# Kernel tuning notes

Hardware: AMD Instinct MI355X
Metric: run time of the kernel (lower is better)

The kernel has to match this reference:

```python
import jax, jax.numpy as jnp
import numpy as np
import math

B, L, H, NH, DH = 2, 2048, 1024, 16, 64  # batch, seq, hidden, heads, head dim


def setup_inputs() -> dict:
    key = jax.random.key(0)
    ks = jax.random.split(key, 12)
    s = 0.02
    return {
        "v": jax.random.normal(ks[0], (B, L, H), jnp.float32),
        "k": jax.random.normal(ks[1], (B, L, H), jnp.float32),
        "q": jax.random.normal(ks[2], (B, L, H), jnp.float32),
        "mask": jnp.zeros((B, 1, 1, L), jnp.bool_),
        "Wv": jax.random.normal(ks[3], (H, H), jnp.float32) * s,
        "bv": jnp.zeros((H,), jnp.float32),
        "Wk": jax.random.normal(ks[4], (H, H), jnp.float32) * s,
        "bk": jnp.zeros((H,), jnp.float32),
        "Wq": jax.random.normal(ks[5], (H, H), jnp.float32) * s,
        "bq": jnp.zeros((H,), jnp.float32),
        "Wt": jax.random.normal(ks[6], (H, 1), jnp.float32) * s,
        "bt": jnp.zeros((1,), jnp.float32),
        "Wm": jax.random.normal(ks[7], (H, H), jnp.float32) * s,
        "bm": jnp.zeros((H,), jnp.float32),
    }


def reference(v, k, q, mask, Wv, bv, Wk, bk, Wq, bq, Wt, bt, Wm, bm):
    vp = (v @ Wv + bv).reshape(B, L, NH, DH).transpose(0, 2, 1, 3)  # [B,NH,L,DH]
    kp = k @ Wk + bk  # [B,L,H]
    qp = q @ Wq + bq  # [B,L,H]
    threshold = (qp * kp) @ Wt + bt  # [B,L,1] learned per-position gate threshold
    kh = kp.reshape(B, L, NH, DH).transpose(0, 2, 1, 3)  # [B,NH,L,DH]
    qh = qp.reshape(B, L, NH, DH).transpose(0, 2, 1, 3)
    scores = jnp.einsum("bhqd,bhkd->bhqk", qh, kh) / math.sqrt(DH)
    scores = jnp.where(mask, -1e9, scores)
    att_map = jax.nn.softmax(scores, axis=-1)  # [B,NH,Lq,Lk]
    # column sums: over queries (axis -2) then over heads -> [B,Lk,1]
    colsum = att_map.sum(axis=2).sum(axis=1)[..., None]
    a = (colsum - threshold) > 0  # [B,L,1] boolean gate
    atted = jnp.einsum("bhqk,bhkd->bhqd", att_map, vp)  # [B,NH,L,DH]
    atted = atted.transpose(0, 2, 1, 3).reshape(B, L, H)
    atted = atted * a.astype(atted.dtype)
    return atted @ Wm + bm
```

## Files before the change

### kernel.cpp

```cpp
#include <hip/hip_runtime.h>
#include <math.h>

#define BATCH 2
#define SEQ   2048
#define HID   1024
#define NHEAD 16
#define DHEAD 64
#define MROWS (BATCH*SEQ)
#define QK_SCALE 0.125f

typedef __attribute__((ext_vector_type(8))) short short8;
typedef __attribute__((ext_vector_type(4))) short short4v;
typedef __attribute__((ext_vector_type(4))) float floatx4;
#define MFMA16(a,b,c) __builtin_amdgcn_mfma_f32_16x16x32_bf16(a,b,c,0,0,0)

__device__ __forceinline__ unsigned short f2bf(float x) {
    union { float f; unsigned u; } v; v.f = x;
    return (unsigned short)((v.u + 0x8000u) >> 16);
}
__device__ __forceinline__ float bf2f(unsigned short s) {
    union { unsigned u; float f; } v; v.u = ((unsigned)s) << 16;
    return v.f;
}
__device__ __forceinline__ unsigned pack_bf16(float lo, float hi) {
    union { float f; unsigned u; } a, b; a.f = lo; b.f = hi;
    return __builtin_amdgcn_perm(b.u + 0x8000u, a.u + 0x8000u, 0x07060302u);
}

__global__ __launch_bounds__(256) void cvt_bf16_kernel(
    const float* __restrict__ i0, const float* __restrict__ i1,
    const float* __restrict__ i2,
    unsigned short* __restrict__ o0, unsigned short* __restrict__ o1,
    unsigned short* __restrict__ o2)
{
    const float* in; unsigned short* out;
    switch (blockIdx.y) {
        case 0:  in = i0; out = o0; break;
        case 1:  in = i1; out = o1; break;
        default: in = i2; out = o2; break;
    }
    const size_t i = ((size_t)blockIdx.x * 256 + threadIdx.x) * 8;
    const float4 a = *(const float4*)&in[i];
    const float4 b = *(const float4*)&in[i + 4];
    uint4 u;
    u.x = pack_bf16(a.x, a.y); u.y = pack_bf16(a.z, a.w);
    u.z = pack_bf16(b.x, b.y); u.w = pack_bf16(b.z, b.w);
    *(uint4*)&out[i] = u;
}

__global__ __launch_bounds__(256) void wtrans_kernel(
    const float* __restrict__ W0, const float* __restrict__ W1,
    const float* __restrict__ W2, const float* __restrict__ W3,
    unsigned short* __restrict__ T0, unsigned short* __restrict__ T1,
    unsigned short* __restrict__ T2, unsigned short* __restrict__ T3)
{
    const float* W; unsigned short* Wt;
    switch (blockIdx.z) {
        case 0: W = W0; Wt = T0; break;
        case 1: W = W1; Wt = T1; break;
        case 2: W = W2; Wt = T2; break;
        default: W = W3; Wt = T3; break;
    }
    __shared__ float T[64][68];
    const int tid = threadIdx.x;
    const int k0 = blockIdx.x * 64, n0 = blockIdx.y * 64;
#pragma unroll
    for (int it = 0; it < 4; it++) {
        const int id = it * 256 + tid;
        const int r = id >> 4, c4 = (id & 15) << 2;
        *(float4*)&T[r][c4] = *(const float4*)&W[(size_t)(k0 + r) * HID + n0 + c4];
    }
    __syncthreads();
#pragma unroll
    for (int it = 0; it < 2; it++) {
        const int id = it * 256 + tid;
        const int n = id >> 3, k8 = (id & 7) << 3;
        uint4 u;
        u.x = pack_bf16(T[k8 + 0][n], T[k8 + 1][n]);
        u.y = pack_bf16(T[k8 + 2][n], T[k8 + 3][n]);
        u.z = pack_bf16(T[k8 + 4][n], T[k8 + 5][n]);
        u.w = pack_bf16(T[k8 + 6][n], T[k8 + 7][n]);
        *(uint4*)&Wt[(size_t)(n0 + n) * HID + k0 + k8] = u;
    }
}

__global__ __launch_bounds__(256) void vtrans_kernel(
    const unsigned short* __restrict__ vb, unsigned short* __restrict__ vt)
{
    __shared__ unsigned short T[64][72];
    const int b = blockIdx.z, h = blockIdx.y, l0 = blockIdx.x * 64;
    const int tid = threadIdx.x;
#pragma unroll
    for (int it = 0; it < 2; it++) {
        const int id = it * 256 + tid;
        const int l = id >> 3, c8 = (id & 7) << 3;
        *(uint4*)&T[l][c8] =
            *(const uint4*)&vb[(size_t)(b * SEQ + l0 + l) * HID + h * DHEAD + c8];
    }
    __syncthreads();
#pragma unroll
    for (int it = 0; it < 2; it++) {
        const int id = it * 256 + tid;
        const int d = id >> 3, l8 = (id & 7) << 3;
        ushort4 u0, u1;
        u0.x = T[l8 + 0][d]; u0.y = T[l8 + 1][d];
        u0.z = T[l8 + 2][d]; u0.w = T[l8 + 3][d];
        u1.x = T[l8 + 4][d]; u1.y = T[l8 + 5][d];
        u1.z = T[l8 + 6][d]; u1.w = T[l8 + 7][d];
        const size_t o = ((size_t)(b * NHEAD + h) * DHEAD + d) * SEQ + l0 + l8;
        *(ushort4*)&vt[o] = u0;
        *(ushort4*)&vt[o + 4] = u1;
    }
}

__global__ __launch_bounds__(256) void gemm_mfma_kernel(
    const unsigned short* __restrict__ Ab, const unsigned short* __restrict__ Bt,
    const float* __restrict__ bias,
    const float* __restrict__ gate_cs, const float* __restrict__ gate_th,
    float* __restrict__ Cf, unsigned short* __restrict__ Cb,
    int M, int N, int K)
{
    __shared__ unsigned short As[128][72];
    __shared__ unsigned short Bs[128][72];
    const int tid = threadIdx.x;
    const int w = tid >> 6, lane = tid & 63;
    const int c = lane & 15, quad = lane >> 4;
    const int m0 = blockIdx.x * 128, n0 = blockIdx.y * 128;
    const int wm = (w >> 1) * 64, wn = (w & 1) * 64;

    bool grow[4] = {true, true, true, true};
    if (gate_cs) {
#pragma unroll
        for (int it = 0; it < 4; it++) {
            const int r = (it * 256 + tid) >> 3;
            grow[it] = (gate_cs[m0 + r] - gate_th[m0 + r]) > 0.f;
        }
    }

    floatx4 acc[4][4];
#pragma unroll
    for (int i = 0; i < 4; i++)
#pragma unroll
        for (int j = 0; j < 4; j++) acc[i][j] = (floatx4){0.f, 0.f, 0.f, 0.f};

    for (int kc = 0; kc < K; kc += 64) {
        __syncthreads();
#pragma unroll
        for (int it = 0; it < 4; it++) {
            const int id = it * 256 + tid;
            const int r = id >> 3, c8 = (id & 7) << 3;
            uint4 u = *(const uint4*)&Ab[(size_t)(m0 + r) * K + kc + c8];
            if (!grow[it]) { u.x = 0; u.y = 0; u.z = 0; u.w = 0; }
            *(uint4*)&As[r][c8] = u;
            *(uint4*)&Bs[r][c8] = *(const uint4*)&Bt[(size_t)(n0 + r) * K + kc + c8];
        }
        __syncthreads();
#pragma unroll
        for (int kk = 0; kk < 2; kk++) {
            short8 af[4], bf[4];
#pragma unroll
            for (int mt = 0; mt < 4; mt++)
                af[mt] = *(const short8*)&As[wm + mt * 16 + c][kk * 32 + quad * 8];
#pragma unroll
            for (int nt = 0; nt < 4; nt++)
                bf[nt] = *(const short8*)&Bs[wn + nt * 16 + c][kk * 32 + quad * 8];
#pragma unroll
            for (int mt = 0; mt < 4; mt++)
#pragma unroll
                for (int nt = 0; nt < 4; nt++)
                    acc[mt][nt] = MFMA16(af[mt], bf[nt], acc[mt][nt]);
        }
    }

#pragma unroll
    for (int nt = 0; nt < 4; nt++) {
        const int n = n0 + wn + nt * 16 + c;
        const float bb = bias[n];
#pragma unroll
        for (int mt = 0; mt < 4; mt++) {
            const int m = m0 + wm + mt * 16 + quad * 4;
#pragma unroll
            for (int r = 0; r < 4; r++) {
                const float val = acc[mt][nt][r] + bb;
                const size_t off = (size_t)(m + r) * N + n;
                if (Cf) Cf[off] = val;
                if (Cb) Cb[off] = f2bf(val);
            }
        }
    }
}

__global__ __launch_bounds__(256) void threshold_kernel(
    const unsigned short* __restrict__ qb, const unsigned short* __restrict__ kb,
    const float* __restrict__ Wt, const float* __restrict__ bt,
    float* __restrict__ thr)
{
    const int w = threadIdx.x >> 6, lane = threadIdx.x & 63;
    const int row = blockIdx.x * 4 + w;
    const unsigned short* qr = qb + (size_t)row * HID;
    const unsigned short* kr = kb + (size_t)row * HID;
    float s = 0.f;
#pragma unroll
    for (int ii = 0; ii < 2; ii++) {
        const int base = ii * 512 + lane * 8;
        const ushort4 q0 = *(const ushort4*)&qr[base];
        const ushort4 q1 = *(const ushort4*)&qr[base + 4];
        const ushort4 k0 = *(const ushort4*)&kr[base];
        const ushort4 k1 = *(const ushort4*)&kr[base + 4];
        const float4 w0 = *(const float4*)&Wt[base];
        const float4 w1 = *(const float4*)&Wt[base + 4];
        s += bf2f(q0.x) * bf2f(k0.x) * w0.x + bf2f(q0.y) * bf2f(k0.y) * w0.y +
             bf2f(q0.z) * bf2f(k0.z) * w0.z + bf2f(q0.w) * bf2f(k0.w) * w0.w +
             bf2f(q1.x) * bf2f(k1.x) * w1.x + bf2f(q1.y) * bf2f(k1.y) * w1.y +
             bf2f(q1.z) * bf2f(k1.z) * w1.z + bf2f(q1.w) * bf2f(k1.w) * w1.w;
    }
#pragma unroll
    for (int off = 32; off > 0; off >>= 1) s += __shfl_xor(s, off, 64);
    if (lane == 0) thr[row] = s + bt[0];
}

__global__ __launch_bounds__(512) void flash_mfma_kernel(
    const unsigned short* __restrict__ qb, const unsigned short* __restrict__ kb,
    const unsigned short* __restrict__ vt, const unsigned char* __restrict__ mask,
    unsigned short* __restrict__ att, float* __restrict__ zinv_out)
{
    const int b = blockIdx.z, h = blockIdx.y;
    const int q0 = blockIdx.x * 128;
    const int tid = threadIdx.x;
    const int w = tid >> 6, lane = tid & 63;
    const int c = lane & 15, quad = lane >> 4;

    __shared__ unsigned short Qs[128][72];
    __shared__ unsigned short Ks[64][72];
    __shared__ unsigned short Vs[64][72];
    __shared__ unsigned short Ps[8][16][68];
    __shared__ float mbf[64];

    const size_t hoff = (size_t)h * DHEAD;
#pragma unroll
    for (int it = 0; it < 2; it++) {
        const int g = it * 512 + tid;
        const int r = g >> 3, c8 = (g & 7) << 3;
        *(uint4*)&Qs[r][c8] =
            *(const uint4*)&qb[(size_t)(b * SEQ + q0 + r) * HID + hoff + c8];
    }
    __syncthreads();
    const short8 aq0 = *(const short8*)&Qs[w * 16 + c][quad * 8];
    const short8 aq1 = *(const short8*)&Qs[w * 16 + c][32 + quad * 8];

    floatx4 acc_o[4];
#pragma unroll
    for (int dt = 0; dt < 4; dt++) acc_o[dt] = (floatx4){0.f, 0.f, 0.f, 0.f};
    float zp[4] = {0.f, 0.f, 0.f, 0.f};
    const size_t vtbase = (size_t)(b * NHEAD + h) * DHEAD * SEQ;

    for (int kc = 0; kc < SEQ; kc += 64) {
        __syncthreads();
        {
            const int r = tid >> 3, c8 = (tid & 7) << 3;
            *(uint4*)&Ks[r][c8] =
                *(const uint4*)&kb[(size_t)(b * SEQ + kc + r) * HID + hoff + c8];
            *(uint4*)&Vs[r][c8] =
                *(const uint4*)&vt[vtbase + (size_t)r * SEQ + kc + c8];
        }
        if (tid < 64) mbf[tid] = mask[(size_t)b * SEQ + kc + tid] ? -1e9f : 0.f;
        __syncthreads();

#pragma unroll
        for (int nt = 0; nt < 4; nt++) {
            const short8 bk0 = *(const short8*)&Ks[nt * 16 + c][quad * 8];
            const short8 bk1 = *(const short8*)&Ks[nt * 16 + c][32 + quad * 8];
            floatx4 s = (floatx4){0.f, 0.f, 0.f, 0.f};
            s = MFMA16(aq0, bk0, s);
            s = MFMA16(aq1, bk1, s);
            const float mb = mbf[nt * 16 + c];
#pragma unroll
            for (int r = 0; r < 4; r++) {
                const float p = __expf(fmaf(s[r], QK_SCALE, mb));
                zp[r] += p;
                Ps[w][quad * 4 + r][nt * 16 + c] = f2bf(p);
            }
        }

        short4v p00 = *(const short4v*)&Ps[w][c][quad * 8];
        short4v p01 = *(const short4v*)&Ps[w][c][quad * 8 + 4];
        short4v p10 = *(const short4v*)&Ps[w][c][32 + quad * 8];
        short4v p11 = *(const short4v*)&Ps[w][c][32 + quad * 8 + 4];
        const short8 ap0 = __builtin_shufflevector(p00, p01, 0, 1, 2, 3, 4, 5, 6, 7);
        const short8 ap1 = __builtin_shufflevector(p10, p11, 0, 1, 2, 3, 4, 5, 6, 7);
#pragma unroll
        for (int dt = 0; dt < 4; dt++) {
            const short8 bv0 = *(const short8*)&Vs[dt * 16 + c][quad * 8];
            const short8 bv1 = *(const short8*)&Vs[dt * 16 + c][32 + quad * 8];
            acc_o[dt] = MFMA16(ap0, bv0, acc_o[dt]);
            acc_o[dt] = MFMA16(ap1, bv1, acc_o[dt]);
        }
    }

#pragma unroll
    for (int r = 0; r < 4; r++) {
        float z = zp[r];
        z += __shfl_xor(z, 1, 64); z += __shfl_xor(z, 2, 64);
        z += __shfl_xor(z, 4, 64); z += __shfl_xor(z, 8, 64);
        zp[r] = 1.0f / (z + 1e-30f);
    }

#pragma unroll
    for (int dt = 0; dt < 4; dt++)
#pragma unroll
        for (int r = 0; r < 4; r++)
            att[(size_t)(b * SEQ + q0 + w * 16 + quad * 4 + r) * HID + hoff +
                dt * 16 + c] = f2bf(acc_o[dt][r] * zp[r]);

    if (c == 0) {
        const size_t zb = (size_t)(b * NHEAD + h) * SEQ + q0 + w * 16 + quad * 4;
#pragma unroll
        for (int r = 0; r < 4; r++) zinv_out[zb + r] = zp[r];
    }
}

__global__ __launch_bounds__(512) void colsum_mfma_kernel(
    const unsigned short* __restrict__ qb, const unsigned short* __restrict__ kb,
    const unsigned char* __restrict__ mask, const float* __restrict__ zinv,
    float* __restrict__ colsum)
{
    const int b = blockIdx.z, h = blockIdx.y, k0 = blockIdx.x * 128;
    const int tid = threadIdx.x;
    const int w = tid >> 6, lane = tid & 63;
    const int c = lane & 15, quad = lane >> 4;

    __shared__ unsigned short Ks[128][72];
    __shared__ unsigned short Qs[64][72];
    __shared__ float zs[64];

    const size_t hoff = (size_t)h * DHEAD;
#pragma unroll
    for (int it = 0; it < 2; it++) {
        const int g = it * 512 + tid;
        const int r = g >> 3, c8 = (g & 7) << 3;
        *(uint4*)&Ks[r][c8] =
            *(const uint4*)&kb[(size_t)(b * SEQ + k0 + r) * HID + hoff + c8];
    }
    float mb[4];
#pragma unroll
    for (int r = 0; r < 4; r++)
        mb[r] = mask[(size_t)b * SEQ + k0 + w * 16 + quad * 4 + r] ? -1e9f : 0.f;
    __syncthreads();
    const short8 ak0 = *(const short8*)&Ks[w * 16 + c][quad * 8];
    const short8 ak1 = *(const short8*)&Ks[w * 16 + c][32 + quad * 8];

    float cs[4] = {0.f, 0.f, 0.f, 0.f};
    const size_t zbase = (size_t)(b * NHEAD + h) * SEQ;

    for (int qc = 0; qc < SEQ; qc += 64) {
        __syncthreads();
        {
            const int r = tid >> 3, c8 = (tid & 7) << 3;
            *(uint4*)&Qs[r][c8] =
                *(const uint4*)&qb[(size_t)(b * SEQ + qc + r) * HID + hoff + c8];
        }
        if (tid < 64) zs[tid] = zinv[zbase + qc + tid];
        __syncthreads();

#pragma unroll
        for (int qt = 0; qt < 4; qt++) {
            const short8 bq0 = *(const short8*)&Qs[qt * 16 + c][quad * 8];
            const short8 bq1 = *(const short8*)&Qs[qt * 16 + c][32 + quad * 8];
            floatx4 s = (floatx4){0.f, 0.f, 0.f, 0.f};
            s = MFMA16(ak0, bq0, s);
            s = MFMA16(ak1, bq1, s);
            const float zi = zs[qt * 16 + c];
#pragma unroll
            for (int r = 0; r < 4; r++)
                cs[r] += __expf(fmaf(s[r], QK_SCALE, mb[r])) * zi;
        }
    }

#pragma unroll
    for (int r = 0; r < 4; r++) {
        float v = cs[r];
        v += __shfl_xor(v, 1, 64); v += __shfl_xor(v, 2, 64);
        v += __shfl_xor(v, 4, 64); v += __shfl_xor(v, 8, 64);
        if (c == 0)
            atomicAdd(&colsum[(size_t)b * SEQ + k0 + w * 16 + quad * 4 + r], v);
    }
}

extern "C" void kernel_launch(void* const* d_in, const int* in_sizes, int n_in,
                              void* d_out, int out_size, void* d_ws, size_t ws_size,
                              hipStream_t stream)
{
    const float* v  = (const float*)d_in[0];
    const float* k  = (const float*)d_in[1];
    const float* q  = (const float*)d_in[2];
    const unsigned char* mask = (const unsigned char*)d_in[3];
    const float* Wv = (const float*)d_in[4];
    const float* bv = (const float*)d_in[5];
    const float* Wk = (const float*)d_in[6];
    const float* bk = (const float*)d_in[7];
    const float* Wq = (const float*)d_in[8];
    const float* bq = (const float*)d_in[9];
    const float* Wt = (const float*)d_in[10];
    const float* bt = (const float*)d_in[11];
    const float* Wm = (const float*)d_in[12];
    const float* bm = (const float*)d_in[13];
    float* out = (float*)d_out;

    const size_t NE = (size_t)MROWS * HID;
    const size_t WE = (size_t)HID * HID;
    unsigned short* qa   = (unsigned short*)d_ws;
    unsigned short* ka   = qa  + NE;
    unsigned short* va   = ka  + NE;
    unsigned short* qp   = va  + NE;
    unsigned short* kp   = qp  + NE;
    unsigned short* vp   = kp  + NE;
    unsigned short* WqT  = vp  + NE;
    unsigned short* WkT  = WqT + WE;
    unsigned short* WvT  = WkT + WE;
    unsigned short* WmT  = WvT + WE;
    float* thr    = (float*)(WmT + WE);
    float* zinv   = thr  + MROWS;
    float* colsum = zinv + (size_t)BATCH * NHEAD * SEQ;
    unsigned short* attb = qa;
    unsigned short* vtb  = ka;

    wtrans_kernel<<<dim3(HID / 64, HID / 64, 4), 256, 0, stream>>>(
        Wq, Wk, Wv, Wm, WqT, WkT, WvT, WmT);

    cvt_bf16_kernel<<<dim3((unsigned)(NE / (256 * 8)), 3), 256, 0, stream>>>(
        q, k, v, qa, ka, va);

    const dim3 gg(MROWS / 128, HID / 128);
    gemm_mfma_kernel<<<gg, 256, 0, stream>>>(qa, WqT, bq, nullptr, nullptr,
                                             nullptr, qp, MROWS, HID, HID);
    gemm_mfma_kernel<<<gg, 256, 0, stream>>>(ka, WkT, bk, nullptr, nullptr,
                                             nullptr, kp, MROWS, HID, HID);
    gemm_mfma_kernel<<<gg, 256, 0, stream>>>(va, WvT, bv, nullptr, nullptr,
                                             nullptr, vp, MROWS, HID, HID);

    vtrans_kernel<<<dim3(SEQ / 64, NHEAD, BATCH), 256, 0, stream>>>(vp, vtb);

    threshold_kernel<<<MROWS / 4, 256, 0, stream>>>(qp, kp, Wt, bt, thr);

    flash_mfma_kernel<<<dim3(SEQ / 128, NHEAD, BATCH), 512, 0, stream>>>(
        qp, kp, vtb, mask, attb, zinv);

    hipMemsetAsync(colsum, 0, MROWS * sizeof(float), stream);
    colsum_mfma_kernel<<<dim3(SEQ / 128, NHEAD, BATCH), 512, 0, stream>>>(
        qp, kp, mask, zinv, colsum);

    gemm_mfma_kernel<<<gg, 256, 0, stream>>>(attb, WmT, bm, colsum, thr,
                                             out, nullptr, MROWS, HID, HID);
}
```

Before: 340.9 us.

## Give each wave two query subtiles, remap blocks per XCD, use native exp2

```diff
diff --git a/kernel.cpp b/kernel.cpp
--- a/kernel.cpp
+++ b/kernel.cpp
@@ -7,12 +7,15 @@
 #define NHEAD 16
 #define DHEAD 64
 #define MROWS (BATCH*SEQ)
-#define QK_SCALE 0.125f
+#define SCALE_LOG2E 0.1803368801111244f
 
 typedef __attribute__((ext_vector_type(8))) short short8;
 typedef __attribute__((ext_vector_type(4))) short short4v;
 typedef __attribute__((ext_vector_type(4))) float floatx4;
 #define MFMA16(a,b,c) __builtin_amdgcn_mfma_f32_16x16x32_bf16(a,b,c,0,0,0)
+
+extern "C" __device__ float __ocml_native_exp2_f32(float);
+#define EXP2F(x) __ocml_native_exp2_f32(x)
 
 __device__ __forceinline__ unsigned short f2bf(float x) {
     union { float f; unsigned u; } v; v.f = x;
@@ -219,48 +222,62 @@
     if (lane == 0) thr[row] = s + bt[0];
 }
 
-__global__ __launch_bounds__(512) void flash_mfma_kernel(
+__global__ __launch_bounds__(256) void flash_mfma_kernel(
     const unsigned short* __restrict__ qb, const unsigned short* __restrict__ kb,
     const unsigned short* __restrict__ vt, const unsigned char* __restrict__ mask,
     unsigned short* __restrict__ att, float* __restrict__ zinv_out)
 {
-    const int b = blockIdx.z, h = blockIdx.y;
-    const int q0 = blockIdx.x * 128;
+    const int n = blockIdx.x;
+    const int xcd = n & 7, t = n >> 3;
+    const int g = xcd + 8 * (t >> 4);
+    const int qblk = t & 15;
+    const int h = g & 15, b = g >> 4;
+    const int q0 = qblk * 128;
+
     const int tid = threadIdx.x;
     const int w = tid >> 6, lane = tid & 63;
     const int c = lane & 15, quad = lane >> 4;
 
-    __shared__ unsigned short Qs[128][72];
-    __shared__ unsigned short Ks[64][72];
-    __shared__ unsigned short Vs[64][72];
-    __shared__ unsigned short Ps[8][16][68];
-    __shared__ float mbf[64];
+    __shared__ unsigned short SM[18048];
+    unsigned short* Ks = SM;
+    unsigned short* Vs = SM + 4608;
+    unsigned short* Ps = SM + 9216;
+    float* mbf = (float*)(SM + 17920);
+    unsigned short* Qs = SM;
 
     const size_t hoff = (size_t)h * DHEAD;
 #pragma unroll
-    for (int it = 0; it < 2; it++) {
-        const int g = it * 512 + tid;
-        const int r = g >> 3, c8 = (g & 7) << 3;
-        *(uint4*)&Qs[r][c8] =
+    for (int it = 0; it < 4; it++) {
+        const int id = it * 256 + tid;
+        const int r = id >> 3, c8 = (id & 7) << 3;
+        *(uint4*)&Qs[r * 72 + c8] =
             *(const uint4*)&qb[(size_t)(b * SEQ + q0 + r) * HID + hoff + c8];
     }
     __syncthreads();
-    const short8 aq0 = *(const short8*)&Qs[w * 16 + c][quad * 8];
-    const short8 aq1 = *(const short8*)&Qs[w * 16 + c][32 + quad * 8];
-
-    floatx4 acc_o[4];
-#pragma unroll
-    for (int dt = 0; dt < 4; dt++) acc_o[dt] = (floatx4){0.f, 0.f, 0.f, 0.f};
-    float zp[4] = {0.f, 0.f, 0.f, 0.f};
+    short8 aq[2][2];
+#pragma unroll
+    for (int s = 0; s < 2; s++) {
+        aq[s][0] = *(const short8*)&Qs[(w * 32 + s * 16 + c) * 72 + quad * 8];
+        aq[s][1] = *(const short8*)&Qs[(w * 32 + s * 16 + c) * 72 + 32 + quad * 8];
+    }
+
+    floatx4 acc[2][4];
+#pragma unroll
+    for (int s = 0; s < 2; s++)
+#pragma unroll
+        for (int dt = 0; dt < 4; dt++) acc[s][dt] = (floatx4){0.f, 0.f, 0.f, 0.f};
+    float zp[2][4] = {{0.f, 0.f, 0.f, 0.f}, {0.f, 0.f, 0.f, 0.f}};
     const size_t vtbase = (size_t)(b * NHEAD + h) * DHEAD * SEQ;
 
     for (int kc = 0; kc < SEQ; kc += 64) {
         __syncthreads();
-        {
-            const int r = tid >> 3, c8 = (tid & 7) << 3;
-            *(uint4*)&Ks[r][c8] =
+#pragma unroll
+        for (int it = 0; it < 2; it++) {
+            const int id = it * 256 + tid;
+            const int r = id >> 3, c8 = (id & 7) << 3;
+            *(uint4*)&Ks[r * 72 + c8] =
                 *(const uint4*)&kb[(size_t)(b * SEQ + kc + r) * HID + hoff + c8];
-            *(uint4*)&Vs[r][c8] =
+            *(uint4*)&Vs[r * 72 + c8] =
                 *(const uint4*)&vt[vtbase + (size_t)r * SEQ + kc + c8];
         }
         if (tid < 64) mbf[tid] = mask[(size_t)b * SEQ + kc + tid] ? -1e9f : 0.f;
@@ -268,95 +285,121 @@
 
 #pragma unroll
         for (int nt = 0; nt < 4; nt++) {
-            const short8 bk0 = *(const short8*)&Ks[nt * 16 + c][quad * 8];
-            const short8 bk1 = *(const short8*)&Ks[nt * 16 + c][32 + quad * 8];
-            floatx4 s = (floatx4){0.f, 0.f, 0.f, 0.f};
-            s = MFMA16(aq0, bk0, s);
-            s = MFMA16(aq1, bk1, s);
+            const short8 bk0 = *(const short8*)&Ks[(nt * 16 + c) * 72 + quad * 8];
+            const short8 bk1 = *(const short8*)&Ks[(nt * 16 + c) * 72 + 32 + quad * 8];
             const float mb = mbf[nt * 16 + c];
 #pragma unroll
-            for (int r = 0; r < 4; r++) {
-                const float p = __expf(fmaf(s[r], QK_SCALE, mb));
-                zp[r] += p;
-                Ps[w][quad * 4 + r][nt * 16 + c] = f2bf(p);
+            for (int s = 0; s < 2; s++) {
+                floatx4 sv = (floatx4){0.f, 0.f, 0.f, 0.f};
+                sv = MFMA16(aq[s][0], bk0, sv);
+                sv = MFMA16(aq[s][1], bk1, sv);
+#pragma unroll
+                for (int r = 0; r < 4; r++) {
+                    const float p = EXP2F(fmaf(sv[r], SCALE_LOG2E, mb));
+                    zp[s][r] += p;
+                    Ps[((2 * w + s) * 16 + quad * 4 + r) * 68 + nt * 16 + c] = f2bf(p);
+                }
             }
         }
 
-        short4v p00 = *(const short4v*)&Ps[w][c][quad * 8];
-        short4v p01 = *(const short4v*)&Ps[w][c][quad * 8 + 4];
-        short4v p10 = *(const short4v*)&Ps[w][c][32 + quad * 8];
-        short4v p11 = *(const short4v*)&Ps[w][c][32 + quad * 8 + 4];
-        const short8 ap0 = __builtin_shufflevector(p00, p01, 0, 1, 2, 3, 4, 5, 6, 7);
-        const short8 ap1 = __builtin_shufflevector(p10, p11, 0, 1, 2, 3, 4, 5, 6, 7);
+        short8 ap[2][2];
+#pragma unroll
+        for (int s = 0; s < 2; s++) {
+            const unsigned short* pr = &Ps[((2 * w + s) * 16 + c) * 68];
+            short4v p00 = *(const short4v*)&pr[quad * 8];
+            short4v p01 = *(const short4v*)&pr[quad * 8 + 4];
+            short4v p10 = *(const short4v*)&pr[32 + quad * 8];
+            short4v p11 = *(const short4v*)&pr[32 + quad * 8 + 4];
+            ap[s][0] = __builtin_shufflevector(p00, p01, 0, 1, 2, 3, 4, 5, 6, 7);
+            ap[s][1] = __builtin_shufflevector(p10, p11, 0, 1, 2, 3, 4, 5, 6, 7);
+        }
 #pragma unroll
         for (int dt = 0; dt < 4; dt++) {
-            const short8 bv0 = *(const short8*)&Vs[dt * 16 + c][quad * 8];
-            const short8 bv1 = *(const short8*)&Vs[dt * 16 + c][32 + quad * 8];
-            acc_o[dt] = MFMA16(ap0, bv0, acc_o[dt]);
-            acc_o[dt] = MFMA16(ap1, bv1, acc_o[dt]);
-        }
-    }
-
-#pragma unroll
-    for (int r = 0; r < 4; r++) {
-        float z = zp[r];
-        z += __shfl_xor(z, 1, 64); z += __shfl_xor(z, 2, 64);
-        z += __shfl_xor(z, 4, 64); z += __shfl_xor(z, 8, 64);
-        zp[r] = 1.0f / (z + 1e-30f);
-    }
-
-#pragma unroll
-    for (int dt = 0; dt < 4; dt++)
-#pragma unroll
-        for (int r = 0; r < 4; r++)
-            att[(size_t)(b * SEQ + q0 + w * 16 + quad * 4 + r) * HID + hoff +
-                dt * 16 + c] = f2bf(acc_o[dt][r] * zp[r]);
-
-    if (c == 0) {
-        const size_t zb = (size_t)(b * NHEAD + h) * SEQ + q0 + w * 16 + quad * 4;
-#pragma unroll
-        for (int r = 0; r < 4; r++) zinv_out[zb + r] = zp[r];
-    }
-}
-
-__global__ __launch_bounds__(512) void colsum_mfma_kernel(
+            const short8 bv0 = *(const short8*)&Vs[(dt * 16 + c) * 72 + quad * 8];
+            const short8 bv1 = *(const short8*)&Vs[(dt * 16 + c) * 72 + 32 + quad * 8];
+#pragma unroll
+            for (int s = 0; s < 2; s++) {
+                acc[s][dt] = MFMA16(ap[s][0], bv0, acc[s][dt]);
+                acc[s][dt] = MFMA16(ap[s][1], bv1, acc[s][dt]);
+            }
+        }
+    }
+
+#pragma unroll
+    for (int s = 0; s < 2; s++) {
+#pragma unroll
+        for (int r = 0; r < 4; r++) {
+            float z = zp[s][r];
+            z += __shfl_xor(z, 1, 64); z += __shfl_xor(z, 2, 64);
+            z += __shfl_xor(z, 4, 64); z += __shfl_xor(z, 8, 64);
+            zp[s][r] = 1.0f / (z + 1e-30f);
+        }
+#pragma unroll
+        for (int dt = 0; dt < 4; dt++)
+#pragma unroll
+            for (int r = 0; r < 4; r++)
+                att[(size_t)(b * SEQ + q0 + w * 32 + s * 16 + quad * 4 + r) * HID +
+                    hoff + dt * 16 + c] = f2bf(acc[s][dt][r] * zp[s][r]);
+        if (c == 0) {
+            const size_t zb = (size_t)(b * NHEAD + h) * SEQ + q0 + w * 32 + s * 16 +
+                              quad * 4;
+#pragma unroll
+            for (int r = 0; r < 4; r++) zinv_out[zb + r] = zp[s][r];
+        }
+    }
+}
+
+__global__ __launch_bounds__(256) void colsum_mfma_kernel(
     const unsigned short* __restrict__ qb, const unsigned short* __restrict__ kb,
     const unsigned char* __restrict__ mask, const float* __restrict__ zinv,
     float* __restrict__ colsum)
 {
-    const int b = blockIdx.z, h = blockIdx.y, k0 = blockIdx.x * 128;
+    const int n = blockIdx.x;
+    const int xcd = n & 7, t = n >> 3;
+    const int g = xcd + 8 * (t >> 4);
+    const int h = g & 15, b = g >> 4;
+    const int k0 = (t & 15) * 128;
+
     const int tid = threadIdx.x;
     const int w = tid >> 6, lane = tid & 63;
     const int c = lane & 15, quad = lane >> 4;
 
-    __shared__ unsigned short Ks[128][72];
-    __shared__ unsigned short Qs[64][72];
-    __shared__ float zs[64];
+    __shared__ unsigned short SM[9216];
+    unsigned short* Qs = SM;
+    float* zs = (float*)(SM + 4608);
+    unsigned short* Kst = SM;
 
     const size_t hoff = (size_t)h * DHEAD;
 #pragma unroll
-    for (int it = 0; it < 2; it++) {
-        const int g = it * 512 + tid;
-        const int r = g >> 3, c8 = (g & 7) << 3;
-        *(uint4*)&Ks[r][c8] =
+    for (int it = 0; it < 4; it++) {
+        const int id = it * 256 + tid;
+        const int r = id >> 3, c8 = (id & 7) << 3;
+        *(uint4*)&Kst[r * 72 + c8] =
             *(const uint4*)&kb[(size_t)(b * SEQ + k0 + r) * HID + hoff + c8];
     }
-    float mb[4];
-#pragma unroll
-    for (int r = 0; r < 4; r++)
-        mb[r] = mask[(size_t)b * SEQ + k0 + w * 16 + quad * 4 + r] ? -1e9f : 0.f;
     __syncthreads();
-    const short8 ak0 = *(const short8*)&Ks[w * 16 + c][quad * 8];
-    const short8 ak1 = *(const short8*)&Ks[w * 16 + c][32 + quad * 8];
-
-    float cs[4] = {0.f, 0.f, 0.f, 0.f};
+    short8 ak[2][2];
+    float mb[2][4];
+#pragma unroll
+    for (int s = 0; s < 2; s++) {
+        ak[s][0] = *(const short8*)&Kst[(w * 32 + s * 16 + c) * 72 + quad * 8];
+        ak[s][1] = *(const short8*)&Kst[(w * 32 + s * 16 + c) * 72 + 32 + quad * 8];
+#pragma unroll
+        for (int r = 0; r < 4; r++)
+            mb[s][r] = mask[(size_t)b * SEQ + k0 + w * 32 + s * 16 + quad * 4 + r]
+                       ? -1e9f : 0.f;
+    }
+
+    float cs[2][4] = {{0.f, 0.f, 0.f, 0.f}, {0.f, 0.f, 0.f, 0.f}};
     const size_t zbase = (size_t)(b * NHEAD + h) * SEQ;
 
     for (int qc = 0; qc < SEQ; qc += 64) {
         __syncthreads();
-        {
-            const int r = tid >> 3, c8 = (tid & 7) << 3;
-            *(uint4*)&Qs[r][c8] =
+#pragma unroll
+        for (int it = 0; it < 2; it++) {
+            const int id = it * 256 + tid;
+            const int r = id >> 3, c8 = (id & 7) << 3;
+            *(uint4*)&Qs[r * 72 + c8] =
                 *(const uint4*)&qb[(size_t)(b * SEQ + qc + r) * HID + hoff + c8];
         }
         if (tid < 64) zs[tid] = zinv[zbase + qc + tid];
@@ -364,26 +407,32 @@
 
 #pragma unroll
         for (int qt = 0; qt < 4; qt++) {
-            const short8 bq0 = *(const short8*)&Qs[qt * 16 + c][quad * 8];
-            const short8 bq1 = *(const short8*)&Qs[qt * 16 + c][32 + quad * 8];
-            floatx4 s = (floatx4){0.f, 0.f, 0.f, 0.f};
-            s = MFMA16(ak0, bq0, s);
-            s = MFMA16(ak1, bq1, s);
+            const short8 bq0 = *(const short8*)&Qs[(qt * 16 + c) * 72 + quad * 8];
+            const short8 bq1 = *(const short8*)&Qs[(qt * 16 + c) * 72 + 32 + quad * 8];
             const float zi = zs[qt * 16 + c];
 #pragma unroll
-            for (int r = 0; r < 4; r++)
-                cs[r] += __expf(fmaf(s[r], QK_SCALE, mb[r])) * zi;
-        }
-    }
-
-#pragma unroll
-    for (int r = 0; r < 4; r++) {
-        float v = cs[r];
-        v += __shfl_xor(v, 1, 64); v += __shfl_xor(v, 2, 64);
-        v += __shfl_xor(v, 4, 64); v += __shfl_xor(v, 8, 64);
-        if (c == 0)
-            atomicAdd(&colsum[(size_t)b * SEQ + k0 + w * 16 + quad * 4 + r], v);
-    }
+            for (int s = 0; s < 2; s++) {
+                floatx4 sv = (floatx4){0.f, 0.f, 0.f, 0.f};
+                sv = MFMA16(ak[s][0], bq0, sv);
+                sv = MFMA16(ak[s][1], bq1, sv);
+#pragma unroll
+                for (int r = 0; r < 4; r++)
+                    cs[s][r] += EXP2F(fmaf(sv[r], SCALE_LOG2E, mb[s][r])) * zi;
+            }
+        }
+    }
+
+#pragma unroll
+    for (int s = 0; s < 2; s++)
+#pragma unroll
+        for (int r = 0; r < 4; r++) {
+            float v = cs[s][r];
+            v += __shfl_xor(v, 1, 64); v += __shfl_xor(v, 2, 64);
+            v += __shfl_xor(v, 4, 64); v += __shfl_xor(v, 8, 64);
+            if (c == 0)
+                atomicAdd(&colsum[(size_t)b * SEQ + k0 + w * 32 + s * 16 +
+                                  quad * 4 + r], v);
+        }
 }
 
 extern "C" void kernel_launch(void* const* d_in, const int* in_sizes, int n_in,
@@ -442,11 +491,11 @@
 
     threshold_kernel<<<MROWS / 4, 256, 0, stream>>>(qp, kp, Wt, bt, thr);
 
-    flash_mfma_kernel<<<dim3(SEQ / 128, NHEAD, BATCH), 512, 0, stream>>>(
+    flash_mfma_kernel<<<BATCH * NHEAD * (SEQ / 128), 256, 0, stream>>>(
         qp, kp, vtb, mask, attb, zinv);
 
     hipMemsetAsync(colsum, 0, MROWS * sizeof(float), stream);
-    colsum_mfma_kernel<<<dim3(SEQ / 128, NHEAD, BATCH), 512, 0, stream>>>(
+    colsum_mfma_kernel<<<BATCH * NHEAD * (SEQ / 128), 256, 0, stream>>>(
         qp, kp, mask, zinv, colsum);
 
     gemm_mfma_kernel<<<gg, 256, 0, stream>>>(attb, WmT, bm, colsum, thr,
```

Result: slower. 357.6 us (+4.9%).
